# Optimization experiments

Hardware: AMD Instinct MI355X
Metric: run time of the kernel (lower is better)

## Reference

```python
import jax, jax.numpy as jnp
import numpy as np


def setup_inputs() -> dict:
    key = jax.random.key(0)
    ks = jax.random.split(key, 4)
    N, T, D, H = 64, 512, 1024, 1024
    x = jax.random.normal(ks[0], (N, T, D), dtype=jnp.float32)
    h0 = jax.random.normal(ks[1], (N, H), dtype=jnp.float32)
    Wx = jax.random.normal(ks[2], (D, 4 * H), dtype=jnp.float32) / np.sqrt(D)
    Wh = jax.random.normal(ks[3], (H, 4 * H), dtype=jnp.float32) / np.sqrt(H)
    b = jnp.zeros((4 * H,), dtype=jnp.float32)
    return {"x": x, "h0": h0, "Wx": Wx, "Wh": Wh, "b": b}


def reference(x, h0, Wx, Wh, b):
    # x: [N, T, D]; h0: [N, H]; Wx: [D, 4H]; Wh: [H, 4H]; b: [4H]
    H = h0.shape[1]
    # Batch the input-to-hidden matmul over all timesteps at once: [N, T, 4H]
    xW = jnp.einsum('ntd,df->ntf', x, Wx) + b
    c0 = jnp.zeros_like(h0)

    def step(carry, xw_t):
        prev_h, prev_c = carry
        preact = xw_t + prev_h @ Wh           # [N, 4H]
        ai, af, ao, ag = jnp.split(preact, 4, axis=1)
        i = jax.nn.sigmoid(ai)
        f = jax.nn.sigmoid(af)
        o = jax.nn.sigmoid(ao)
        g = jnp.tanh(ag)
        next_c = f * prev_c + i * g
        next_h = o * jnp.tanh(next_c)
        return (next_h, next_c), next_h

    # scan over time: move T to leading axis
    _, hs = jax.lax.scan(step, (h0, c0), jnp.swapaxes(xW, 0, 1))
    return jnp.swapaxes(hs, 0, 1)  # [N, T, H]
```

## Files before the change

### kernel.cpp

```cpp
#include <hip/hip_runtime.h>
#include <cstdint>
#include <cstddef>

#define N_ 64
#define T_ 512
#define D_ 1024
#define H_ 1024
#define FH 4096

typedef __attribute__((ext_vector_type(8))) short bf16x8;
typedef __attribute__((ext_vector_type(4))) float f32x4;

static __device__ __forceinline__ uint16_t f2bf_(float f) {
  union { float f; uint32_t u; } v; v.f = f;
  uint32_t u = v.u + 0x7FFFu + ((v.u >> 16) & 1u);
  return (uint16_t)(u >> 16);
}
static __device__ __forceinline__ float bf2f_(uint16_t s) {
  union { uint32_t u; float f; } v; v.u = ((uint32_t)s) << 16;
  return v.f;
}
static __device__ __forceinline__ void unpk2_(unsigned long long e,
                                              uint32_t& hi, uint32_t& lo) {
  uint32_t a = (uint32_t)e, b = (uint32_t)(e >> 32);
  hi = (a >> 16) | (b & 0xFFFF0000u);
  lo = (a & 0xFFFFu) | (b << 16);
}

#define ALD(p) (*(p))

__global__ __launch_bounds__(256) void pack_w_k(const float* __restrict__ W,
                                                ushort* __restrict__ hi,
                                                ushort* __restrict__ lo) {
  const int i = blockIdx.x * 256 + threadIdx.x;
  const int lane = i & 63, kc = (i >> 6) & 31, bid = i >> 11;
  const int c = lane & 15;
  const int col = (c >> 2) * H_ + (bid << 2) + (c & 3);
  const int k0 = (kc << 5) + ((lane >> 4) << 3);
  const size_t o = ((size_t)(bid * 32 + kc) * 64 + lane) * 8;
#pragma unroll
  for (int e = 0; e < 8; ++e) {
    float v = W[(size_t)(k0 + e) * FH + col];
    ushort h = f2bf_(v);
    hi[o + e] = h;
    lo[o + e] = f2bf_(v - bf2f_(h));
  }
}

__global__ __launch_bounds__(256) void split_f32_k(const float* __restrict__ src,
                                                   ushort* __restrict__ hi,
                                                   ushort* __restrict__ lo,
                                                   unsigned* bar) {
  if (bar != nullptr && blockIdx.x == 0) {
    bar[threadIdx.x] = 0u;
    bar[256 + threadIdx.x] = 0u;
  }
  const size_t i = (size_t)blockIdx.x * 256 + threadIdx.x;
  float4 v = reinterpret_cast<const float4*>(src)[i];
  ushort4 h, l;
  h.x = f2bf_(v.x); l.x = f2bf_(v.x - bf2f_(h.x));
  h.y = f2bf_(v.y); l.y = f2bf_(v.y - bf2f_(h.y));
  h.z = f2bf_(v.z); l.z = f2bf_(v.z - bf2f_(h.z));
  h.w = f2bf_(v.w); l.w = f2bf_(v.w - bf2f_(h.w));
  reinterpret_cast<ushort4*>(hi)[i] = h;
  reinterpret_cast<ushort4*>(lo)[i] = l;
}

__global__ __launch_bounds__(256) void conv_h0pk_k(const float* __restrict__ src,
                                                   uint32_t* __restrict__ dst) {
  const int i = blockIdx.x * 256 + threadIdx.x;
  float4 v = reinterpret_cast<const float4*>(src)[i];
  uint4 o;
  { ushort h = f2bf_(v.x); o.x = ((uint32_t)h << 16) | f2bf_(v.x - bf2f_(h)); }
  { ushort h = f2bf_(v.y); o.y = ((uint32_t)h << 16) | f2bf_(v.y - bf2f_(h)); }
  { ushort h = f2bf_(v.z); o.z = ((uint32_t)h << 16) | f2bf_(v.z - bf2f_(h)); }
  { ushort h = f2bf_(v.w); o.w = ((uint32_t)h << 16) | f2bf_(v.w - bf2f_(h)); }
  reinterpret_cast<uint4*>(dst)[i] = o;
}

__global__ __launch_bounds__(512, 1) void lstm_persist_mfma(
    const ushort* __restrict__ Whh_g, const ushort* __restrict__ Whl_g,
    const ushort* __restrict__ Wxh, const ushort* __restrict__ Wxl,
    const ushort* __restrict__ xh, const ushort* __restrict__ xl,
    const float* __restrict__ bias,
    uint32_t* __restrict__ hseq,
    float* __restrict__ out, unsigned* __restrict__ bar) {
  extern __shared__ char ldsraw[];
  bf16x8* const WhH = (bf16x8*)ldsraw;
  bf16x8* const WhL = WhH + 2048;
  float* const pre = (float*)(WhL + 2048);
  float (*const xwr)[64][4][4] =
      (float(*)[64][4][4])(pre + 128 * 17);

  const int tid = threadIdx.x, bid = blockIdx.x;
  const int lane = tid & 63, w = tid >> 6;
  const int mt = w & 3, kh = w >> 2;
  const int khb = kh << 4;
  const int arow = (mt << 4) | (lane & 15);
  const int kg = lane >> 4;
  const int dc = lane & 15, dr = (lane >> 4) << 2;
  const int en = tid >> 2, ejj = tid & 3;

  unsigned* const rel = bar + 384;

  float bias4[4] = {0.f, 0.f, 0.f, 0.f};
  float creg = 0.f;
  if (tid < 256) {
#pragma unroll
    for (int g = 0; g < 4; ++g) bias4[g] = bias[g * H_ + (bid << 2) + ejj];
  }

  {
    const bf16x8* gh = reinterpret_cast<const bf16x8*>(Whh_g) + (size_t)bid * 2048;
    const bf16x8* gl = reinterpret_cast<const bf16x8*>(Whl_g) + (size_t)bid * 2048;
#pragma unroll
    for (int r = 0; r < 4; ++r) {
      int u = tid + (r << 9);
      WhH[u] = gh[u];
      WhL[u] = gl[u];
    }
  }
  __syncthreads();

  const bf16x8* Bxh = reinterpret_cast<const bf16x8*>(Wxh) + (size_t)bid * 2048 + lane;
  const bf16x8* Bxl = reinterpret_cast<const bf16x8*>(Wxl) + (size_t)bid * 2048 + lane;

  auto xburst = [&](int tb) {
    const int mt2 = mt;
    const int t0 = tb + (kh << 1);
    const int t1 = t0 + 1;
    const int row = (mt2 << 4) | (lane & 15);
    const ushort* a0h = xh + ((size_t)row * T_ + t0) * D_ + (kg << 3);
    const ushort* a0l = xl + ((size_t)row * T_ + t0) * D_ + (kg << 3);
    const ushort* a1h = xh + ((size_t)row * T_ + t1) * D_ + (kg << 3);
    const ushort* a1l = xl + ((size_t)row * T_ + t1) * D_ + (kg << 3);
    f32x4 xa0 = {0.f, 0.f, 0.f, 0.f};
    f32x4 xa1 = {0.f, 0.f, 0.f, 0.f};
#pragma unroll 4
    for (int kc = 0; kc < 32; ++kc) {
      bf16x8 bh = Bxh[kc << 6];
      bf16x8 bl = Bxl[kc << 6];
      bf16x8 h0 = *reinterpret_cast<const bf16x8*>(a0h + (kc << 5));
      bf16x8 l0 = *reinterpret_cast<const bf16x8*>(a0l + (kc << 5));
      bf16x8 h1 = *reinterpret_cast<const bf16x8*>(a1h + (kc << 5));
      bf16x8 l1 = *reinterpret_cast<const bf16x8*>(a1l + (kc << 5));
      xa0 = __builtin_amdgcn_mfma_f32_16x16x32_bf16(h0, bh, xa0, 0, 0, 0);
      xa1 = __builtin_amdgcn_mfma_f32_16x16x32_bf16(h1, bh, xa1, 0, 0, 0);
      xa0 = __builtin_amdgcn_mfma_f32_16x16x32_bf16(h0, bl, xa0, 0, 0, 0);
      xa1 = __builtin_amdgcn_mfma_f32_16x16x32_bf16(h1, bl, xa1, 0, 0, 0);
      xa0 = __builtin_amdgcn_mfma_f32_16x16x32_bf16(l0, bh, xa0, 0, 0, 0);
      xa1 = __builtin_amdgcn_mfma_f32_16x16x32_bf16(l1, bh, xa1, 0, 0, 0);
    }
    const int g = dc >> 2, jj = dc & 3;
#pragma unroll
    for (int r = 0; r < 4; ++r) {
      const int rw = (mt2 << 4) + dr + r;
      xwr[t0 & 7][rw][jj][g] = xa0[r];
      xwr[t1 & 7][rw][jj][g] = xa1[r];
    }
  };

  xburst(0);
  xburst(4);

  for (int t = 0; t < T_; ++t) {
    {
      f32x4 acc0 = {0.f, 0.f, 0.f, 0.f};
      f32x4 acc1 = {0.f, 0.f, 0.f, 0.f};
      const unsigned long long* Apk =
          (const unsigned long long*)(hseq + (size_t)t * 65536) +
          arow * 512 + kg * 4 + (kh << 8);

      unsigned long long pa0, pa1, pa2, pa3, pb0, pb1, pb2, pb3;
      unsigned long long pc0, pc1, pc2, pc3, pd0, pd1, pd2, pd3;
      unsigned long long qa0, qa1, qa2, qa3, qb0, qb1, qb2, qb3;
      unsigned long long qc0, qc1, qc2, qc3, qd0, qd1, qd2, qd3;

#define HLD(P, CH)                                                            \
  {                                                                           \
    const unsigned long long* ap_ = Apk + ((CH) << 6);                        \
    P##a0 = ALD(ap_ + 0);  P##a1 = ALD(ap_ + 1);                              \
    P##a2 = ALD(ap_ + 2);  P##a3 = ALD(ap_ + 3);                              \
    P##b0 = ALD(ap_ + 16); P##b1 = ALD(ap_ + 17);                             \
    P##b2 = ALD(ap_ + 18); P##b3 = ALD(ap_ + 19);                             \
    P##c0 = ALD(ap_ + 32); P##c1 = ALD(ap_ + 33);                             \
    P##c2 = ALD(ap_ + 34); P##c3 = ALD(ap_ + 35);                             \
    P##d0 = ALD(ap_ + 48); P##d1 = ALD(ap_ + 49);                             \
    P##d2 = ALD(ap_ + 50); P##d3 = ALD(ap_ + 51);                             \
  }

#define HKC(E0, E1, E2, E3, KCG, ACC)                                         \
  {                                                                           \
    union { uint32_t u[4]; bf16x8 v; } fh_, fl_;                              \
    unpk2_(E0, fh_.u[0], fl_.u[0]);                                           \
    unpk2_(E1, fh_.u[1], fl_.u[1]);                                           \
    unpk2_(E2, fh_.u[2], fl_.u[2]);                                           \
    unpk2_(E3, fh_.u[3], fl_.u[3]);                                           \
    bf16x8 bh_ = WhH[((KCG) << 6) + lane];                                    \
    bf16x8 bl_ = WhL[((KCG) << 6) + lane];                                    \
    ACC = __builtin_amdgcn_mfma_f32_16x16x32_bf16(fh_.v, bh_, ACC, 0, 0, 0);  \
    ACC = __builtin_amdgcn_mfma_f32_16x16x32_bf16(fh_.v, bl_, ACC, 0, 0, 0);  \
    ACC = __builtin_amdgcn_mfma_f32_16x16x32_bf16(fl_.v, bh_, ACC, 0, 0, 0);  \
  }

#define HCOMP(P, CH)                                                          \
  HKC(P##a0, P##a1, P##a2, P##a3, khb + (CH) * 4 + 0, acc0)                   \
  HKC(P##b0, P##b1, P##b2, P##b3, khb + (CH) * 4 + 1, acc1)                   \
  HKC(P##c0, P##c1, P##c2, P##c3, khb + (CH) * 4 + 2, acc0)                   \
  HKC(P##d0, P##d1, P##d2, P##d3, khb + (CH) * 4 + 3, acc1)

      HLD(p, 0)
      HLD(q, 1) HCOMP(p, 0)
      HLD(p, 2) HCOMP(q, 1)
      HLD(q, 3) HCOMP(p, 2)
      HCOMP(q, 3)
#undef HLD
#undef HKC
#undef HCOMP

      f32x4 accs = acc0 + acc1;
#pragma unroll
      for (int r = 0; r < 4; ++r)
        pre[((kh << 6) + (mt << 4) + dr + r) * 17 + dc] = accs[r];
    }
    __syncthreads();

    if (tid < 256) {
      const float* xvp = &xwr[t & 7][en][ejj][0];
      float a[4];
#pragma unroll
      for (int g = 0; g < 4; ++g)
        a[g] = pre[en * 17 + (g << 2) + ejj] +
               pre[(64 + en) * 17 + (g << 2) + ejj] + xvp[g] + bias4[g];
      float iv = 1.f / (1.f + __expf(-a[0]));
      float fv = 1.f / (1.f + __expf(-a[1]));
      float ov = 1.f / (1.f + __expf(-a[2]));
      float gv = tanhf(a[3]);
      creg = fmaf(fv, creg, iv * gv);
      float hn = ov * tanhf(creg);
      out[(size_t)en * ((size_t)T_ * H_) + (size_t)t * H_ + (bid << 2) + ejj] = hn;
      ushort hh = f2bf_(hn);
      uint32_t pk = ((uint32_t)hh << 16) | f2bf_(hn - bf2f_(hh));
      __hip_atomic_store(&hseq[(size_t)(t + 1) * 65536 + en * H_ + (bid << 2) + ejj],
                         pk, __ATOMIC_RELAXED, __HIP_MEMORY_SCOPE_AGENT);
    }

    asm volatile("s_waitcnt vmcnt(0)" ::: "memory");
    __syncthreads();

    const unsigned tgt = (unsigned)(t + 1);
    if (tid == 0)
      __hip_atomic_store(&bar[bid], tgt, __ATOMIC_RELAXED,
                         __HIP_MEMORY_SCOPE_AGENT);

    if (t != 0 && (t & 3) == 0 && t + 4 < T_) xburst(t + 4);

    if (bid == 0 && tid < 64) {
      const unsigned long long* fl = (const unsigned long long*)bar;
      for (;;) {
        unsigned long long v0 = __hip_atomic_load(fl + tid, __ATOMIC_RELAXED,
                                                  __HIP_MEMORY_SCOPE_AGENT);
        unsigned long long v1 = __hip_atomic_load(fl + 64 + tid, __ATOMIC_RELAXED,
                                                  __HIP_MEMORY_SCOPE_AGENT);
        bool ok = ((unsigned)v0 >= tgt) && ((unsigned)(v0 >> 32) >= tgt) &&
                  ((unsigned)v1 >= tgt) && ((unsigned)(v1 >> 32) >= tgt);
        if (__all((int)ok)) break;
      }
      if (tid == 0)
        __hip_atomic_store(rel, tgt, __ATOMIC_RELAXED, __HIP_MEMORY_SCOPE_AGENT);
    }
    if (tid == 0) {
      while (__hip_atomic_load(rel, __ATOMIC_RELAXED,
                               __HIP_MEMORY_SCOPE_AGENT) < tgt)
        __builtin_amdgcn_s_sleep(1);
    }
    __syncthreads();
  }
}

__global__ __launch_bounds__(256) void lstm_step_fb(
    const float* __restrict__ xt, const float* __restrict__ Wx,
    const float* __restrict__ Wh, const float* __restrict__ bias,
    const float* __restrict__ h_prev, long long hstride,
    float* __restrict__ cbuf, float* __restrict__ h_out, int first) {
  __shared__ float hS[32][128];
  __shared__ float wT[32][132];
  __shared__ float pre[32][34];
  const int tid = threadIdx.x;
  const int colblk = blockIdx.x & 127;
  const int nh = blockIdx.x >> 7;
  const int j0 = colblk << 3;
  const int n0 = nh << 5;
  const int ng = tid >> 4, cg2 = tid & 15;
  const int na = ng << 1, ca = cg2 << 1;

  float acc[2][2] = {{0.f, 0.f}, {0.f, 0.f}};

#pragma unroll
  for (int pr = 0; pr < 2; ++pr) {
    const float* src = (pr == 0) ? h_prev : xt;
    long long sstr = (pr == 0) ? hstride : (long long)T_ * D_;
    const float* W = (pr == 0) ? Wh : Wx;
    for (int k0 = 0; k0 < 1024; k0 += 128) {
      __syncthreads();
#pragma unroll
      for (int p = 0; p < 4; ++p) {
        int idx = tid + (p << 8);
        int r = idx >> 5, c4 = (idx & 31) << 2;
        *reinterpret_cast<float4*>(&hS[r][c4]) =
            *reinterpret_cast<const float4*>(src + (size_t)(n0 + r) * sstr + k0 + c4);
      }
#pragma unroll
      for (int p = 0; p < 4; ++p) {
        int idx = tid + (p << 8);
        int k = idx >> 3, sub = idx & 7;
        int g = sub >> 1, hf = (sub & 1) << 2;
        float4 v = *reinterpret_cast<const float4*>(
            W + (size_t)(k0 + k) * FH + g * H_ + j0 + hf);
        int cb = (g << 3) + hf;
        wT[cb][k] = v.x; wT[cb + 1][k] = v.y; wT[cb + 2][k] = v.z; wT[cb + 3][k] = v.w;
      }
      __syncthreads();
#pragma unroll
      for (int kk = 0; kk < 128; kk += 4) {
        float4 h0v = *reinterpret_cast<const float4*>(&hS[na][kk]);
        float4 h1v = *reinterpret_cast<const float4*>(&hS[na + 1][kk]);
        float4 w0 = *reinterpret_cast<const float4*>(&wT[ca][kk]);
        float4 w1 = *reinterpret_cast<const float4*>(&wT[ca + 1][kk]);
        acc[0][0] = fmaf(h0v.x, w0.x, acc[0][0]); acc[0][0] = fmaf(h0v.y, w0.y, acc[0][0]);
        acc[0][0] = fmaf(h0v.z, w0.z, acc[0][0]); acc[0][0] = fmaf(h0v.w, w0.w, acc[0][0]);
        acc[0][1] = fmaf(h0v.x, w1.x, acc[0][1]); acc[0][1] = fmaf(h0v.y, w1.y, acc[0][1]);
        acc[0][1] = fmaf(h0v.z, w1.z, acc[0][1]); acc[0][1] = fmaf(h0v.w, w1.w, acc[0][1]);
        acc[1][0] = fmaf(h1v.x, w0.x, acc[1][0]); acc[1][0] = fmaf(h1v.y, w0.y, acc[1][0]);
        acc[1][0] = fmaf(h1v.z, w0.z, acc[1][0]); acc[1][0] = fmaf(h1v.w, w0.w, acc[1][0]);
        acc[1][1] = fmaf(h1v.x, w1.x, acc[1][1]); acc[1][1] = fmaf(h1v.y, w1.y, acc[1][1]);
        acc[1][1] = fmaf(h1v.z, w1.z, acc[1][1]); acc[1][1] = fmaf(h1v.w, w1.w, acc[1][1]);
      }
    }
  }

  pre[na][ca] = acc[0][0];
  pre[na][ca + 1] = acc[0][1];
  pre[na + 1][ca] = acc[1][0];
  pre[na + 1][ca + 1] = acc[1][1];
  __syncthreads();

  const int nl = tid >> 3, jl = tid & 7;
  const int n = n0 + nl;
  const int jg = j0 + jl;
  float ai = pre[nl][jl] + bias[jg];
  float af = pre[nl][8 + jl] + bias[H_ + jg];
  float ao = pre[nl][16 + jl] + bias[2 * H_ + jg];
  float ag = pre[nl][24 + jl] + bias[3 * H_ + jg];
  float cp = first ? 0.0f : cbuf[n * H_ + jg];
  float iv = 1.f / (1.f + __expf(-ai));
  float fv = 1.f / (1.f + __expf(-af));
  float ov = 1.f / (1.f + __expf(-ao));
  float gv = tanhf(ag);
  float cn = fmaf(fv, cp, iv * gv);
  cbuf[n * H_ + jg] = cn;
  h_out[(size_t)n * ((size_t)T_ * H_) + jg] = ov * tanhf(cn);
}

extern "C" void kernel_launch(void* const* d_in, const int* in_sizes, int n_in,
                              void* d_out, int out_size, void* d_ws, size_t ws_size,
                              hipStream_t stream) {
  (void)in_sizes; (void)n_in; (void)out_size;
  const float* x  = (const float*)d_in[0];
  const float* h0 = (const float*)d_in[1];
  const float* Wx = (const float*)d_in[2];
  const float* Wh = (const float*)d_in[3];
  const float* b  = (const float*)d_in[4];
  float* out = (float*)d_out;

  const size_t MB = 1u << 20;
  char* p = (char*)d_ws;

  if (ws_size >= 300 * MB) {
    unsigned* bar = (unsigned*)p;
    ushort* Whh = (ushort*)(p + 1 * MB);
    ushort* Whl = (ushort*)(p + 9 * MB);
    ushort* Wxh = (ushort*)(p + 17 * MB);
    ushort* Wxl = (ushort*)(p + 25 * MB);
    uint32_t* hseq = (uint32_t*)(p + 33 * MB);
    ushort* xh = (ushort*)(p + 168 * MB);
    ushort* xl = (ushort*)(p + 232 * MB);

    pack_w_k<<<dim3(2048), dim3(256), 0, stream>>>(Wh, Whh, Whl);
    pack_w_k<<<dim3(2048), dim3(256), 0, stream>>>(Wx, Wxh, Wxl);
    split_f32_k<<<dim3(32768), dim3(256), 0, stream>>>(x, xh, xl, bar);
    conv_h0pk_k<<<dim3(64), dim3(256), 0, stream>>>(h0, hseq);

    const unsigned SH = 65536 + 128 * 17 * 4 + 8 * 64 * 16 * 4;
    hipFuncSetAttribute((const void*)lstm_persist_mfma,
                        hipFuncAttributeMaxDynamicSharedMemorySize, (int)SH);
    lstm_persist_mfma<<<dim3(256), dim3(512), SH, stream>>>(
        Whh, Whl, Wxh, Wxl, xh, xl, b, hseq, out, bar);
  } else {
    float* cbuf = (float*)p;
    for (int t = 0; t < T_; ++t) {
      const float* hp = (t == 0) ? h0 : out + (size_t)(t - 1) * H_;
      long long hstr = (t == 0) ? (long long)H_ : (long long)T_ * H_;
      lstm_step_fb<<<dim3(256), dim3(256), 0, stream>>>(
          x + (size_t)t * D_, Wx, Wh, b, hp, hstr, cbuf,
          out + (size_t)t * H_, t == 0);
    }
  }
}
```

Measured before the change: 9.110 ms.

## Hoist input projection into separate chunked MFMA GEMM kernels before the recurrent scan

```diff
diff --git a/kernel.cpp b/kernel.cpp
--- a/kernel.cpp
+++ b/kernel.cpp
@@ -25,6 +25,18 @@
   uint32_t a = (uint32_t)e, b = (uint32_t)(e >> 32);
   hi = (a >> 16) | (b & 0xFFFF0000u);
   lo = (a & 0xFFFFu) | (b << 16);
+}
+static __device__ __forceinline__ void cvt8_(const float* p, bf16x8& hv,
+                                             bf16x8& lv) {
+  float4 v0 = *reinterpret_cast<const float4*>(p);
+  float4 v1 = *reinterpret_cast<const float4*>(p + 4);
+  float f[8] = {v0.x, v0.y, v0.z, v0.w, v1.x, v1.y, v1.z, v1.w};
+#pragma unroll
+  for (int e = 0; e < 8; ++e) {
+    ushort h = f2bf_(f[e]);
+    hv[e] = (short)h;
+    lv[e] = (short)f2bf_(f[e] - bf2f_(h));
+  }
 }
 
 #define ALD(p) (*(p))
@@ -47,27 +59,13 @@
   }
 }
 
-__global__ __launch_bounds__(256) void split_f32_k(const float* __restrict__ src,
-                                                   ushort* __restrict__ hi,
-                                                   ushort* __restrict__ lo,
+__global__ __launch_bounds__(256) void conv_h0pk_k(const float* __restrict__ src,
+                                                   uint32_t* __restrict__ dst,
                                                    unsigned* bar) {
-  if (bar != nullptr && blockIdx.x == 0) {
+  if (blockIdx.x == 0) {
     bar[threadIdx.x] = 0u;
-    bar[256 + threadIdx.x] = 0u;
-  }
-  const size_t i = (size_t)blockIdx.x * 256 + threadIdx.x;
-  float4 v = reinterpret_cast<const float4*>(src)[i];
-  ushort4 h, l;
-  h.x = f2bf_(v.x); l.x = f2bf_(v.x - bf2f_(h.x));
-  h.y = f2bf_(v.y); l.y = f2bf_(v.y - bf2f_(h.y));
-  h.z = f2bf_(v.z); l.z = f2bf_(v.z - bf2f_(h.z));
-  h.w = f2bf_(v.w); l.w = f2bf_(v.w - bf2f_(h.w));
-  reinterpret_cast<ushort4*>(hi)[i] = h;
-  reinterpret_cast<ushort4*>(lo)[i] = l;
-}
-
-__global__ __launch_bounds__(256) void conv_h0pk_k(const float* __restrict__ src,
-                                                   uint32_t* __restrict__ dst) {
+    if (threadIdx.x < 8) bar[384 + 32 * threadIdx.x] = 0u;
+  }
   const int i = blockIdx.x * 256 + threadIdx.x;
   float4 v = reinterpret_cast<const float4*>(src)[i];
   uint4 o;
@@ -78,19 +76,73 @@
   reinterpret_cast<uint4*>(dst)[i] = o;
 }
 
-__global__ __launch_bounds__(512, 1) void lstm_persist_mfma(
+__global__ __launch_bounds__(256) void gemm_xw_mfma(
+    const ushort* __restrict__ Wxh, const ushort* __restrict__ Wxl,
+    const float* __restrict__ x, const float* __restrict__ bias,
+    uint32_t* __restrict__ xwp, int tb) {
+  const int bid = blockIdx.x;
+  const int tl = blockIdx.y << 2;
+  const int t0 = tb + tl;
+  const int tid = threadIdx.x, lane = tid & 63, mt = tid >> 6;
+  const int row = (mt << 4) | (lane & 15);
+  const int kg = lane >> 4;
+
+  const bf16x8* Bh = reinterpret_cast<const bf16x8*>(Wxh) + (size_t)bid * 2048 + lane;
+  const bf16x8* Bl = reinterpret_cast<const bf16x8*>(Wxl) + (size_t)bid * 2048 + lane;
+  const float* ax = x + ((size_t)row * T_ + t0) * D_ + (kg << 3);
+
+  f32x4 xa0 = {0.f, 0.f, 0.f, 0.f};
+  f32x4 xa1 = {0.f, 0.f, 0.f, 0.f};
+  f32x4 xa2 = {0.f, 0.f, 0.f, 0.f};
+  f32x4 xa3 = {0.f, 0.f, 0.f, 0.f};
+#pragma unroll 2
+  for (int kc = 0; kc < 32; ++kc) {
+    bf16x8 bh = Bh[kc << 6];
+    bf16x8 bl = Bl[kc << 6];
+    bf16x8 h0, l0, h1, l1, h2, l2, h3, l3;
+    cvt8_(ax + (kc << 5), h0, l0);
+    cvt8_(ax + D_ + (kc << 5), h1, l1);
+    cvt8_(ax + 2 * D_ + (kc << 5), h2, l2);
+    cvt8_(ax + 3 * D_ + (kc << 5), h3, l3);
+    xa0 = __builtin_amdgcn_mfma_f32_16x16x32_bf16(h0, bh, xa0, 0, 0, 0);
+    xa1 = __builtin_amdgcn_mfma_f32_16x16x32_bf16(h1, bh, xa1, 0, 0, 0);
+    xa2 = __builtin_amdgcn_mfma_f32_16x16x32_bf16(h2, bh, xa2, 0, 0, 0);
+    xa3 = __builtin_amdgcn_mfma_f32_16x16x32_bf16(h3, bh, xa3, 0, 0, 0);
+    xa0 = __builtin_amdgcn_mfma_f32_16x16x32_bf16(h0, bl, xa0, 0, 0, 0);
+    xa1 = __builtin_amdgcn_mfma_f32_16x16x32_bf16(h1, bl, xa1, 0, 0, 0);
+    xa2 = __builtin_amdgcn_mfma_f32_16x16x32_bf16(h2, bl, xa2, 0, 0, 0);
+    xa3 = __builtin_amdgcn_mfma_f32_16x16x32_bf16(h3, bl, xa3, 0, 0, 0);
+    xa0 = __builtin_amdgcn_mfma_f32_16x16x32_bf16(l0, bh, xa0, 0, 0, 0);
+    xa1 = __builtin_amdgcn_mfma_f32_16x16x32_bf16(l1, bh, xa1, 0, 0, 0);
+    xa2 = __builtin_amdgcn_mfma_f32_16x16x32_bf16(l2, bh, xa2, 0, 0, 0);
+    xa3 = __builtin_amdgcn_mfma_f32_16x16x32_bf16(l3, bh, xa3, 0, 0, 0);
+  }
+
+  const int dc = lane & 15, dr = (lane >> 4) << 2;
+  const int g = dc >> 2, jj = dc & 3;
+  const float bv = bias[g * H_ + (bid << 2) + jj];
+#pragma unroll
+  for (int r = 0; r < 4; ++r) {
+    const int rw = (mt << 4) + dr + r;
+    const size_t o = ((size_t)tl * 256 + bid) * 1024 + rw * 16 + jj * 4 + g;
+    float v0 = xa0[r] + bv, v1 = xa1[r] + bv, v2 = xa2[r] + bv, v3 = xa3[r] + bv;
+    ushort h;
+    h = f2bf_(v0); xwp[o] = ((uint32_t)h << 16) | f2bf_(v0 - bf2f_(h));
+    h = f2bf_(v1); xwp[o + 262144] = ((uint32_t)h << 16) | f2bf_(v1 - bf2f_(h));
+    h = f2bf_(v2); xwp[o + 2 * 262144] = ((uint32_t)h << 16) | f2bf_(v2 - bf2f_(h));
+    h = f2bf_(v3); xwp[o + 3 * 262144] = ((uint32_t)h << 16) | f2bf_(v3 - bf2f_(h));
+  }
+}
+
+__global__ __launch_bounds__(512, 2) void lstm_scan_k(
     const ushort* __restrict__ Whh_g, const ushort* __restrict__ Whl_g,
-    const ushort* __restrict__ Wxh, const ushort* __restrict__ Wxl,
-    const ushort* __restrict__ xh, const ushort* __restrict__ xl,
-    const float* __restrict__ bias,
-    uint32_t* __restrict__ hseq,
-    float* __restrict__ out, unsigned* __restrict__ bar) {
+    const uint32_t* __restrict__ xwp,
+    uint32_t* __restrict__ hseq, float* __restrict__ cbuf,
+    float* __restrict__ out, unsigned* __restrict__ bar, int tb) {
   extern __shared__ char ldsraw[];
   bf16x8* const WhH = (bf16x8*)ldsraw;
   bf16x8* const WhL = WhH + 2048;
   float* const pre = (float*)(WhL + 2048);
-  float (*const xwr)[64][4][4] =
-      (float(*)[64][4][4])(pre + 128 * 17);
 
   const int tid = threadIdx.x, bid = blockIdx.x;
   const int lane = tid & 63, w = tid >> 6;
@@ -101,14 +153,7 @@
   const int dc = lane & 15, dr = (lane >> 4) << 2;
   const int en = tid >> 2, ejj = tid & 3;
 
-  unsigned* const rel = bar + 384;
-
-  float bias4[4] = {0.f, 0.f, 0.f, 0.f};
-  float creg = 0.f;
-  if (tid < 256) {
-#pragma unroll
-    for (int g = 0; g < 4; ++g) bias4[g] = bias[g * H_ + (bid << 2) + ejj];
-  }
+  unsigned* const relmy = bar + 384 + ((bid & 7) << 5);
 
   {
     const bf16x8* gh = reinterpret_cast<const bf16x8*>(Whh_g) + (size_t)bid * 2048;
@@ -122,59 +167,18 @@
   }
   __syncthreads();
 
-  const bf16x8* Bxh = reinterpret_cast<const bf16x8*>(Wxh) + (size_t)bid * 2048 + lane;
-  const bf16x8* Bxl = reinterpret_cast<const bf16x8*>(Wxl) + (size_t)bid * 2048 + lane;
-
-  auto xburst = [&](int tb) {
-    const int mt2 = mt;
-    const int t0 = tb + (kh << 1);
-    const int t1 = t0 + 1;
-    const int row = (mt2 << 4) | (lane & 15);
-    const ushort* a0h = xh + ((size_t)row * T_ + t0) * D_ + (kg << 3);
-    const ushort* a0l = xl + ((size_t)row * T_ + t0) * D_ + (kg << 3);
-    const ushort* a1h = xh + ((size_t)row * T_ + t1) * D_ + (kg << 3);
-    const ushort* a1l = xl + ((size_t)row * T_ + t1) * D_ + (kg << 3);
-    f32x4 xa0 = {0.f, 0.f, 0.f, 0.f};
-    f32x4 xa1 = {0.f, 0.f, 0.f, 0.f};
-#pragma unroll 4
-    for (int kc = 0; kc < 32; ++kc) {
-      bf16x8 bh = Bxh[kc << 6];
-      bf16x8 bl = Bxl[kc << 6];
-      bf16x8 h0 = *reinterpret_cast<const bf16x8*>(a0h + (kc << 5));
-      bf16x8 l0 = *reinterpret_cast<const bf16x8*>(a0l + (kc << 5));
-      bf16x8 h1 = *reinterpret_cast<const bf16x8*>(a1h + (kc << 5));
-      bf16x8 l1 = *reinterpret_cast<const bf16x8*>(a1l + (kc << 5));
-      xa0 = __builtin_amdgcn_mfma_f32_16x16x32_bf16(h0, bh, xa0, 0, 0, 0);
-      xa1 = __builtin_amdgcn_mfma_f32_16x16x32_bf16(h1, bh, xa1, 0, 0, 0);
-      xa0 = __builtin_amdgcn_mfma_f32_16x16x32_bf16(h0, bl, xa0, 0, 0, 0);
-      xa1 = __builtin_amdgcn_mfma_f32_16x16x32_bf16(h1, bl, xa1, 0, 0, 0);
-      xa0 = __builtin_amdgcn_mfma_f32_16x16x32_bf16(l0, bh, xa0, 0, 0, 0);
-      xa1 = __builtin_amdgcn_mfma_f32_16x16x32_bf16(l1, bh, xa1, 0, 0, 0);
-    }
-    const int g = dc >> 2, jj = dc & 3;
-#pragma unroll
-    for (int r = 0; r < 4; ++r) {
-      const int rw = (mt2 << 4) + dr + r;
-      xwr[t0 & 7][rw][jj][g] = xa0[r];
-      xwr[t1 & 7][rw][jj][g] = xa1[r];
-    }
-  };
-
-  xburst(0);
-  xburst(4);
-
-  for (int t = 0; t < T_; ++t) {
-    {
-      f32x4 acc0 = {0.f, 0.f, 0.f, 0.f};
-      f32x4 acc1 = {0.f, 0.f, 0.f, 0.f};
-      const unsigned long long* Apk =
-          (const unsigned long long*)(hseq + (size_t)t * 65536) +
-          arow * 512 + kg * 4 + (kh << 8);
-
-      unsigned long long pa0, pa1, pa2, pa3, pb0, pb1, pb2, pb3;
-      unsigned long long pc0, pc1, pc2, pc3, pd0, pd1, pd2, pd3;
-      unsigned long long qa0, qa1, qa2, qa3, qb0, qb1, qb2, qb3;
-      unsigned long long qc0, qc1, qc2, qc3, qd0, qd1, qd2, qd3;
+  for (int tl = 0; tl < 256; ++tl) {
+    const int t = tb + tl;
+    f32x4 acc0 = {0.f, 0.f, 0.f, 0.f};
+    f32x4 acc1 = {0.f, 0.f, 0.f, 0.f};
+    const unsigned long long* Apk =
+        (const unsigned long long*)(hseq + (size_t)t * 65536) +
+        arow * 512 + (kh << 8) + kg * 4;
+
+    unsigned long long pa0, pa1, pa2, pa3, pb0, pb1, pb2, pb3;
+    unsigned long long pc0, pc1, pc2, pc3, pd0, pd1, pd2, pd3;
+    unsigned long long qa0, qa1, qa2, qa3, qb0, qb1, qb2, qb3;
+    unsigned long long qc0, qc1, qc2, qc3, qd0, qd1, qd2, qd3;
 
 #define HLD(P, CH)                                                            \
   {                                                                           \
@@ -209,40 +213,46 @@
   HKC(P##c0, P##c1, P##c2, P##c3, khb + (CH) * 4 + 2, acc0)                   \
   HKC(P##d0, P##d1, P##d2, P##d3, khb + (CH) * 4 + 3, acc1)
 
-      HLD(p, 0)
-      HLD(q, 1) HCOMP(p, 0)
-      HLD(p, 2) HCOMP(q, 1)
-      HLD(q, 3) HCOMP(p, 2)
-      HCOMP(q, 3)
+    HLD(p, 0)
+    HLD(q, 1) HCOMP(p, 0)
+    HLD(p, 2) HCOMP(q, 1)
+    HLD(q, 3) HCOMP(p, 2)
+    HCOMP(q, 3)
 #undef HLD
 #undef HKC
 #undef HCOMP
 
-      f32x4 accs = acc0 + acc1;
-#pragma unroll
-      for (int r = 0; r < 4; ++r)
-        pre[((kh << 6) + (mt << 4) + dr + r) * 17 + dc] = accs[r];
-    }
+    f32x4 accs = acc0 + acc1;
+#pragma unroll
+    for (int r = 0; r < 4; ++r)
+      pre[((kh << 6) + (mt << 4) + dr + r) * 17 + dc] = accs[r];
     __syncthreads();
 
     if (tid < 256) {
-      const float* xvp = &xwr[t & 7][en][ejj][0];
-      float a[4];
-#pragma unroll
-      for (int g = 0; g < 4; ++g)
-        a[g] = pre[en * 17 + (g << 2) + ejj] +
-               pre[(64 + en) * 17 + (g << 2) + ejj] + xvp[g] + bias4[g];
-      float iv = 1.f / (1.f + __expf(-a[0]));
-      float fv = 1.f / (1.f + __expf(-a[1]));
-      float ov = 1.f / (1.f + __expf(-a[2]));
-      float gv = tanhf(a[3]);
-      creg = fmaf(fv, creg, iv * gv);
-      float hn = ov * tanhf(creg);
+      const uint4 xp = *reinterpret_cast<const uint4*>(
+          xwp + (size_t)tl * 262144 + (size_t)bid * 1024 + en * 16 + ejj * 4);
+      float a0 = pre[en * 17 + ejj] + pre[(64 + en) * 17 + ejj] +
+                 bf2f_((ushort)(xp.x >> 16)) + bf2f_((ushort)(xp.x & 0xFFFF));
+      float a1 = pre[en * 17 + 4 + ejj] + pre[(64 + en) * 17 + 4 + ejj] +
+                 bf2f_((ushort)(xp.y >> 16)) + bf2f_((ushort)(xp.y & 0xFFFF));
+      float a2 = pre[en * 17 + 8 + ejj] + pre[(64 + en) * 17 + 8 + ejj] +
+                 bf2f_((ushort)(xp.z >> 16)) + bf2f_((ushort)(xp.z & 0xFFFF));
+      float a3 = pre[en * 17 + 12 + ejj] + pre[(64 + en) * 17 + 12 + ejj] +
+                 bf2f_((ushort)(xp.w >> 16)) + bf2f_((ushort)(xp.w & 0xFFFF));
+      const int hx = en * H_ + (bid << 2) + ejj;
+      float cp = (t == 0) ? 0.f : cbuf[hx];
+      float iv = 1.f / (1.f + __expf(-a0));
+      float fv = 1.f / (1.f + __expf(-a1));
+      float ov = 1.f / (1.f + __expf(-a2));
+      float gv = tanhf(a3);
+      float cn = fmaf(fv, cp, iv * gv);
+      cbuf[hx] = cn;
+      float hn = ov * tanhf(cn);
       out[(size_t)en * ((size_t)T_ * H_) + (size_t)t * H_ + (bid << 2) + ejj] = hn;
       ushort hh = f2bf_(hn);
       uint32_t pk = ((uint32_t)hh << 16) | f2bf_(hn - bf2f_(hh));
-      __hip_atomic_store(&hseq[(size_t)(t + 1) * 65536 + en * H_ + (bid << 2) + ejj],
-                         pk, __ATOMIC_RELAXED, __HIP_MEMORY_SCOPE_AGENT);
+      __hip_atomic_store(&hseq[(size_t)(t + 1) * 65536 + hx], pk,
+                         __ATOMIC_RELAXED, __HIP_MEMORY_SCOPE_AGENT);
     }
 
     asm volatile("s_waitcnt vmcnt(0)" ::: "memory");
@@ -252,9 +262,6 @@
     if (tid == 0)
       __hip_atomic_store(&bar[bid], tgt, __ATOMIC_RELAXED,
                          __HIP_MEMORY_SCOPE_AGENT);
-
-    if (t != 0 && (t & 3) == 0 && t + 4 < T_) xburst(t + 4);
-
     if (bid == 0 && tid < 64) {
       const unsigned long long* fl = (const unsigned long long*)bar;
       for (;;) {
@@ -266,11 +273,12 @@
                   ((unsigned)v1 >= tgt) && ((unsigned)(v1 >> 32) >= tgt);
         if (__all((int)ok)) break;
       }
-      if (tid == 0)
-        __hip_atomic_store(rel, tgt, __ATOMIC_RELAXED, __HIP_MEMORY_SCOPE_AGENT);
+      if (tid < 8)
+        __hip_atomic_store(bar + 384 + (tid << 5), tgt, __ATOMIC_RELAXED,
+                           __HIP_MEMORY_SCOPE_AGENT);
     }
     if (tid == 0) {
-      while (__hip_atomic_load(rel, __ATOMIC_RELAXED,
+      while (__hip_atomic_load(relmy, __ATOMIC_RELAXED,
                                __HIP_MEMORY_SCOPE_AGENT) < tgt)
         __builtin_amdgcn_s_sleep(1);
     }
@@ -376,26 +384,30 @@
   const size_t MB = 1u << 20;
   char* p = (char*)d_ws;
 
-  if (ws_size >= 300 * MB) {
+  if (ws_size >= 420 * MB) {
     unsigned* bar = (unsigned*)p;
     ushort* Whh = (ushort*)(p + 1 * MB);
     ushort* Whl = (ushort*)(p + 9 * MB);
     ushort* Wxh = (ushort*)(p + 17 * MB);
     ushort* Wxl = (ushort*)(p + 25 * MB);
     uint32_t* hseq = (uint32_t*)(p + 33 * MB);
-    ushort* xh = (ushort*)(p + 168 * MB);
-    ushort* xl = (ushort*)(p + 232 * MB);
+    float* cbuf = (float*)(p + 162 * MB);
+    uint32_t* xwp = (uint32_t*)(p + 163 * MB);
 
     pack_w_k<<<dim3(2048), dim3(256), 0, stream>>>(Wh, Whh, Whl);
     pack_w_k<<<dim3(2048), dim3(256), 0, stream>>>(Wx, Wxh, Wxl);
-    split_f32_k<<<dim3(32768), dim3(256), 0, stream>>>(x, xh, xl, bar);
-    conv_h0pk_k<<<dim3(64), dim3(256), 0, stream>>>(h0, hseq);
-
-    const unsigned SH = 65536 + 128 * 17 * 4 + 8 * 64 * 16 * 4;
-    hipFuncSetAttribute((const void*)lstm_persist_mfma,
+    conv_h0pk_k<<<dim3(64), dim3(256), 0, stream>>>(h0, hseq, bar);
+
+    const unsigned SH = 2048 * 16 * 2 + 128 * 17 * 4;
+    hipFuncSetAttribute((const void*)lstm_scan_k,
                         hipFuncAttributeMaxDynamicSharedMemorySize, (int)SH);
-    lstm_persist_mfma<<<dim3(256), dim3(512), SH, stream>>>(
-        Whh, Whl, Wxh, Wxl, xh, xl, b, hseq, out, bar);
+
+    gemm_xw_mfma<<<dim3(256, 64), dim3(256), 0, stream>>>(Wxh, Wxl, x, b, xwp, 0);
+    lstm_scan_k<<<dim3(256), dim3(512), SH, stream>>>(Whh, Whl, xwp, hseq, cbuf,
+                                                      out, bar, 0);
+    gemm_xw_mfma<<<dim3(256, 64), dim3(256), 0, stream>>>(Wxh, Wxl, x, b, xwp, 256);
+    lstm_scan_k<<<dim3(256), dim3(512), SH, stream>>>(Whh, Whl, xwp, hseq, cbuf,
+                                                      out, bar, 256);
   } else {
     float* cbuf = (float*)p;
     for (int t = 0; t < T_; ++t) {
```

Result: slower. 9.381 ms (+3.0%).
